# Optimization experiments

Measured on AMD Instinct MI355X. Metric: run time of the kernel, lower is better.

The kernel has to match this reference:

```python
import jax, jax.numpy as jnp
import numpy as np

WS = 7        # window size (cubic)
SHIFT = 3     # shift size (cubic)
NH = 6        # num heads
EPS = 1e-5


def _layernorm(x, g, b):
    m = x.mean(-1, keepdims=True)
    v = ((x - m) ** 2).mean(-1, keepdims=True)
    return (x - m) / jnp.sqrt(v + EPS) * g + b


def _win_partition(x, ws):
    # (B,H,W,T,C) -> (B*nW, ws^3, C)
    B, H, W, T, C = x.shape
    x = x.reshape(B, H // ws, ws, W // ws, ws, T // ws, ws, C)
    return x.transpose(0, 1, 3, 5, 2, 4, 6, 7).reshape(-1, ws * ws * ws, C)


def _win_reverse(w, ws, B, H, W, T):
    # (B*nW, ws^3, C) -> (B,H,W,T,C)
    C = w.shape[-1]
    x = w.reshape(B, H // ws, W // ws, T // ws, ws, ws, ws, C)
    return x.transpose(0, 1, 4, 2, 5, 3, 6, 7).reshape(B, H, W, T, C)


def _rel_index(ws):
    # 3D relative position index, (N, N) int, N = ws^3 (torch.meshgrid default 'ij')
    coords = np.stack(np.meshgrid(np.arange(ws), np.arange(ws), np.arange(ws), indexing='ij'))
    cf = coords.reshape(3, -1)
    rel = (cf[:, :, None] - cf[:, None, :]).transpose(1, 2, 0)
    rel[:, :, 0] += ws - 1
    rel[:, :, 1] += ws - 1
    rel[:, :, 2] += ws - 1
    rel[:, :, 0] *= (2 * ws - 1) ** 2
    rel[:, :, 1] *= (2 * ws - 1)
    return rel.sum(-1)


def _compute_mask(Hp, Wp, Tp, ws, shift):
    img = np.zeros((1, Hp, Wp, Tp, 1), np.float32)
    cnt = 0
    sl = (slice(0, -ws), slice(-ws, -shift), slice(-shift, None))
    for h in sl:
        for w in sl:
            for t in sl:
                img[:, h, w, t, :] = cnt
                cnt += 1
    mw = np.asarray(_win_partition(jnp.asarray(img), ws)).reshape(-1, ws ** 3)  # (nW, N)
    am = mw[:, None, :] - mw[:, :, None]
    return jnp.asarray(np.where(am != 0, -100.0, 0.0).astype(np.float32))


def setup_inputs() -> dict:
    key = jax.random.key(0)
    ks = jax.random.split(key, 10)
    B, Hd, Wd, Td, C = 2, 28, 28, 28, 192
    L = Hd * Wd * Td
    Ch = int(C * 4.0)
    s = 0.02
    inp = {
        'x': jax.random.normal(ks[0], (B, L, C), jnp.float32),
        'mask': _compute_mask(Hd, Wd, Td, WS, SHIFT),
        'gamma1': jnp.ones((C,), jnp.float32),
        'beta1': jnp.zeros((C,), jnp.float32),
        'qkv_w': jax.random.normal(ks[1], (3 * C, C), jnp.float32) * s,
        'qkv_b': jnp.zeros((3 * C,), jnp.float32),
        'rpb_table': jax.random.normal(ks[2], ((2 * WS - 1) ** 3, NH), jnp.float32) * s,
        'proj_w': jax.random.normal(ks[3], (C, C), jnp.float32) * s,
        'proj_b': jnp.zeros((C,), jnp.float32),
        'gamma2': jnp.ones((C,), jnp.float32),
        'beta2': jnp.zeros((C,), jnp.float32),
        'fc1_w': jax.random.normal(ks[4], (Ch, C), jnp.float32) * s,
        'fc1_b': jnp.zeros((Ch,), jnp.float32),
        'fc2_w': jax.random.normal(ks[5], (C, Ch), jnp.float32) * s,
        'fc2_b': jnp.zeros((C,), jnp.float32),
        'H': Hd, 'W': Wd, 'T': Td,
    }
    return inp


def reference(x, mask, gamma1, beta1, qkv_w, qkv_b, rpb_table, proj_w, proj_b,
              gamma2, beta2, fc1_w, fc1_b, fc2_w, fc2_b, H, W, T):
    B, L, C = x.shape
    hd = C // NH
    scale = hd ** -0.5
    shortcut = x

    h1 = _layernorm(x, gamma1, beta1).reshape(B, H, W, T, C)
    # H,W,T are multiples of WS -> no padding; cyclic shift for SW-MSA
    shifted = jnp.roll(h1, (-SHIFT, -SHIFT, -SHIFT), axis=(1, 2, 3))
    xw = _win_partition(shifted, WS)            # (B*nW, N, C)
    Bn, N, _ = xw.shape

    qkv = (xw @ qkv_w.T + qkv_b).reshape(Bn, N, 3, NH, hd).transpose(2, 0, 3, 1, 4)
    q, k, v = qkv[0] * scale, qkv[1], qkv[2]     # (Bn, NH, N, hd)
    attn = jnp.einsum('bhnd,bhmd->bhnm', q, k)   # (Bn, NH, N, N)

    idx = _rel_index(WS)
    bias = rpb_table[idx.reshape(-1)].reshape(N, N, NH).transpose(2, 0, 1)
    attn = attn + bias[None]

    nW = mask.shape[0]
    attn = attn.reshape(Bn // nW, nW, NH, N, N) + mask[None, :, None]
    attn = jax.nn.softmax(attn.reshape(Bn, NH, N, N), axis=-1)

    out = jnp.einsum('bhnm,bhmd->bhnd', attn, v).transpose(0, 2, 1, 3).reshape(Bn, N, C)
    out = out @ proj_w.T + proj_b

    shifted = _win_reverse(out, WS, B, H, W, T)
    xr = jnp.roll(shifted, (SHIFT, SHIFT, SHIFT), axis=(1, 2, 3)).reshape(B, L, C)

    x = shortcut + xr
    h2 = _layernorm(x, gamma2, beta2)
    m = jax.nn.gelu(h2 @ fc1_w.T + fc1_b, approximate=False)
    return x + (m @ fc2_w.T + fc2_b)
```

## Files before the change

kernel.cpp:

```cpp
#include <hip/hip_runtime.h>
#include <hip/hip_bf16.h>

typedef unsigned short u16;
typedef unsigned int u32;
typedef __attribute__((ext_vector_type(8))) short s16x8;
typedef __attribute__((ext_vector_type(4))) float f32x4;

__device__ __forceinline__ float bf2f(u16 v) {
    union { u32 u; float f; } x; x.u = ((u32)v) << 16; return x.f;
}
__device__ __forceinline__ u16 f2bf(float f) {
    union { float f; u32 u; } x; x.f = f;
    u32 r = x.u + 0x7fffu + ((x.u >> 16) & 1u);
    return (u16)(r >> 16);
}
__device__ __forceinline__ u32 f2bf_pk(float a, float b) {
    u32 ua = __builtin_bit_cast(u32, a);
    u32 ub = __builtin_bit_cast(u32, b);
    ua += 0x7fffu + ((ua >> 16) & 1u);
    ub += 0x7fffu + ((ub >> 16) & 1u);
    return __builtin_amdgcn_perm(ub, ua, 0x07060302);
}
__device__ __forceinline__ void gl2lds(const u16* g, u16* l) {
    __builtin_amdgcn_global_load_lds(
        (const __attribute__((address_space(1))) unsigned int*)g,
        (__attribute__((address_space(3))) unsigned int*)l, 16, 0, 0);
}

#define L_TOK 21952
#define C_DIM 192
#define LOG2E 1.4426950408889634f
#define Q2SCALE 0.2550565444463649f
#define BT_STR 352

__global__ __launch_bounds__(256) void cvt_k(const float* __restrict__ s0,
                                             const float* __restrict__ s1,
                                             const float* __restrict__ s2,
                                             const float* __restrict__ s3,
                                             u16* __restrict__ dst)
{
    int i = blockIdx.x * 256 + threadIdx.x;
    float v;
    if (i < 110592) v = s0[i];
    else if (i < 147456) v = s1[i - 110592];
    else if (i < 294912) v = s2[i - 147456];
    else v = s3[i - 294912];
    dst[i] = f2bf(v);
}

__global__ __launch_bounds__(256) void bias48_k(const float* __restrict__ rpb,
                                                u16* __restrict__ biasT)
{
    const int n = blockIdx.x * 256 + threadIdx.x;
    if (n >= BT_STR) return;
    const int m = blockIdx.y;
    const int z = blockIdx.z;
    const int hh = z >> 3, wt = z & 7;
    u16 v;
    if (n <= 342 && m <= 342) {
        int hq = n / 49, r1 = n - hq * 49, wq = r1 / 7, tq = r1 - wq * 7;
        int hm = m / 49, r2 = m - hm * 49, wm = r2 / 7, tm = r2 - wm * 7;
        int idx = ((hq - hm + 6) * 13 + (wq - wm + 6)) * 13 + (tq - tm + 6);
        float b = rpb[idx * 6 + hh];
        int rq = ((wt & 4) ? (hq < 4 ? 1 : 2) : 0) * 9
               + ((wt & 2) ? (wq < 4 ? 1 : 2) : 0) * 3
               + ((wt & 1) ? (tq < 4 ? 1 : 2) : 0);
        int rm = ((wt & 4) ? (hm < 4 ? 1 : 2) : 0) * 9
               + ((wt & 2) ? (wm < 4 ? 1 : 2) : 0) * 3
               + ((wt & 1) ? (tm < 4 ? 1 : 2) : 0);
        if (rq != rm) b -= 100.0f;
        v = f2bf(b * LOG2E);
    } else {
        v = f2bf(-100000.0f);
    }
    biasT[((size_t)z * 352 + m) * BT_STR + n] = v;
}

template<int MODE>
__global__ __launch_bounds__(256) void ln_k(const float* __restrict__ in,
                                            const float* __restrict__ g,
                                            const float* __restrict__ b,
                                            u16* __restrict__ out)
{
    const int lane = threadIdx.x & 63, wv = threadIdx.x >> 6;
    const int tok = blockIdx.x * 4 + wv;
    size_t base = (size_t)tok * C_DIM;
    float x0 = in[base + lane];
    float x1 = in[base + 64 + lane];
    float x2 = in[base + 128 + lane];
    float s = x0 + x1 + x2;
    float sq = x0 * x0 + x1 * x1 + x2 * x2;
    #pragma unroll
    for (int off = 32; off > 0; off >>= 1) {
        s += __shfl_xor(s, off, 64);
        sq += __shfl_xor(sq, off, 64);
    }
    const float mean = s * (1.0f / 192.0f);
    float var = sq * (1.0f / 192.0f) - mean * mean;
    var = fmaxf(var, 0.0f);
    const float rstd = rsqrtf(var + 1e-5f);

    size_t obase;
    if (MODE == 0) {
        int bi = tok / L_TOK;
        int l = tok - bi * L_TOK;
        int h = l / 784;
        int rm = l - h * 784;
        int w = rm / 28;
        int t = rm - w * 28;
        int hs = h + 25; if (hs >= 28) hs -= 28;
        int ws = w + 25; if (ws >= 28) ws -= 28;
        int ts = t + 25; if (ts >= 28) ts -= 28;
        int win = ((bi * 4 + hs / 7) * 4 + ws / 7) * 4 + ts / 7;
        int n = (hs % 7) * 49 + (ws % 7) * 7 + (ts % 7);
        obase = ((size_t)win * 343 + n) * C_DIM;
    } else {
        obase = base;
    }
    #pragma unroll
    for (int i = 0; i < 3; i++) {
        int c = lane + i * 64;
        float xv = (i == 0) ? x0 : (i == 1) ? x1 : x2;
        float y = (xv - mean) * rstd * g[c] + b[c];
        out[obase + c] = f2bf(y);
    }
}

template<int K, int EPI>
__global__ __launch_bounds__(256) void gemm_k(const u16* __restrict__ A,
                                              const u16* __restrict__ W,
                                              const float* __restrict__ bias,
                                              void* __restrict__ outp,
                                              const void* __restrict__ resp,
                                              int Ncols)
{
    __shared__ __align__(16) u16 As[3 * 128 * 32];
    __shared__ __align__(16) u16 Bs[3 * 64 * 32];
    const int t = threadIdx.x;
    const int bm = blockIdx.y;
    const int n0 = blockIdx.x * 64;
    const int lane = t & 63, wv = t >> 6;
    const int wm = (wv >> 1) * 64, wn = (wv & 1) * 32;
    const int r16 = lane & 15, quad = lane >> 4;

    f32x4 acc[4][2];
    #pragma unroll
    for (int i = 0; i < 4; i++)
        #pragma unroll
        for (int j = 0; j < 2; j++) acc[i][j] = (f32x4){0.f, 0.f, 0.f, 0.f};

    const int ar = t >> 2, ac = (t & 3) * 8;
    const size_t abase = (size_t)bm * 128 * K;

    for (int kc = 0; kc < K; kc += 96) {
        if (kc) __syncthreads();
        #pragma unroll
        for (int kt = 0; kt < 3; kt++) {
            const int k0 = kc + kt * 32;
            gl2lds(&A[abase + (size_t)ar * K + k0 + ac], &As[kt * 4096 + 8 * t]);
            gl2lds(&A[abase + (size_t)(ar + 64) * K + k0 + ac], &As[kt * 4096 + 2048 + 8 * t]);
            gl2lds(&W[(size_t)(n0 + ar) * K + k0 + ac], &Bs[kt * 2048 + 8 * t]);
        }
        __syncthreads();
        #pragma unroll
        for (int kt = 0; kt < 3; kt++) {
            s16x8 af[4], bf[2];
            #pragma unroll
            for (int fm = 0; fm < 4; fm++)
                af[fm] = *(const s16x8*)&As[kt * 4096 + (wm + fm * 16 + r16) * 32 + quad * 8];
            #pragma unroll
            for (int fn = 0; fn < 2; fn++)
                bf[fn] = *(const s16x8*)&Bs[kt * 2048 + (wn + fn * 16 + r16) * 32 + quad * 8];
            #pragma unroll
            for (int fm = 0; fm < 4; fm++)
                #pragma unroll
                for (int fn = 0; fn < 2; fn++)
                    acc[fm][fn] = __builtin_amdgcn_mfma_f32_16x16x32_bf16(af[fm], bf[fn], acc[fm][fn], 0, 0, 0);
        }
    }

    #pragma unroll
    for (int fm = 0; fm < 4; fm++) {
        #pragma unroll
        for (int fn = 0; fn < 2; fn++) {
            #pragma unroll
            for (int r = 0; r < 4; r++) {
                const int grow = bm * 128 + wm + fm * 16 + quad * 4 + r;
                const int gcol = n0 + wn + fn * 16 + r16;
                float v = acc[fm][fn][r] + bias[gcol];
                if (EPI == 0) {
                    if (gcol < 192) v *= Q2SCALE;
                    ((u16*)outp)[(size_t)grow * Ncols + gcol] = f2bf(v);
                } else if (EPI == 1) {
                    v = 0.5f * v * (1.0f + erff(v * 0.70710678118654752f));
                    ((u16*)outp)[(size_t)grow * Ncols + gcol] = f2bf(v);
                } else if (EPI == 2) {
                    size_t o = (size_t)grow * C_DIM + gcol;
                    ((float*)outp)[o] = v + ((const float*)resp)[o];
                } else {
                    int win = grow / 343, n = grow - win * 343;
                    int bi = win >> 6, wi = win & 63;
                    int hw = wi >> 4, ww = (wi >> 2) & 3, tw = wi & 3;
                    int ph = n / 49, rem = n - ph * 49;
                    int pw = rem / 7, pt = rem - pw * 7;
                    int h = hw * 7 + ph + 3; if (h >= 28) h -= 28;
                    int w = ww * 7 + pw + 3; if (w >= 28) w -= 28;
                    int tt = tw * 7 + pt + 3; if (tt >= 28) tt -= 28;
                    int l = (h * 28 + w) * 28 + tt;
                    size_t o = ((size_t)bi * L_TOK + l) * C_DIM + gcol;
                    ((float*)outp)[o] = v + ((const float*)resp)[o];
                }
            }
        }
    }
}

__global__ __launch_bounds__(256, 3) void attn_k(const u16* __restrict__ qkv,
                                                 const u16* __restrict__ biasAll,
                                                 u16* __restrict__ out)
{
    __shared__ __align__(16) u16 Ks[352 * 32];
    __shared__ __align__(16) u16 Vt[32 * 360];
    __shared__ __align__(16) u16 Pb[4][16 * 40];

    const int hh = blockIdx.x;
    const int win = blockIdx.y;
    const int wi = win & 63;
    const int t = threadIdx.x, lane = t & 63, wv = t >> 6;
    const int r16 = lane & 15, quad = lane >> 4;
    const size_t qbase = (size_t)win * 343 * 576 + hh * 32;

    for (int j = t; j < 343 * 4; j += 256) {
        int m = j >> 2, ch = j & 3;
        *(uint4*)&Ks[m * 32 + ch * 8] = *(const uint4*)&qkv[qbase + (size_t)m * 576 + 192 + ch * 8];
    }
    if (t < 36) {
        int m = 343 + (t >> 2), ch = t & 3;
        *(uint4*)&Ks[m * 32 + ch * 8] = (uint4){0u, 0u, 0u, 0u};
    }
    for (int i = t; i < 343 * 16; i += 256) {
        int m = i >> 4, d2 = (i & 15) * 2;
        int pm = (m & ~31) + 2 * (m & 15) + ((m >> 4) & 1);
        u32 w2 = *(const u32*)&qkv[qbase + (size_t)m * 576 + 384 + d2];
        Vt[d2 * 360 + pm] = (u16)(w2 & 0xffffu);
        Vt[(d2 + 1) * 360 + pm] = (u16)(w2 >> 16);
    }
    for (int i = t; i < 32 * 9; i += 256) {
        int d = i / 9, m = 343 + i % 9;
        int pm = (m & ~31) + 2 * (m & 15) + ((m >> 4) & 1);
        Vt[d * 360 + pm] = 0;
    }
    __syncthreads();

    const int wt = (((wi >> 4) == 3) ? 4 : 0) | ((((wi >> 2) & 3) == 3) ? 2 : 0)
                 | (((wi & 3) == 3) ? 1 : 0);
    const u16* biashT = biasAll + (size_t)(hh * 8 + wt) * 352 * BT_STR;

    for (int qt = 0; qt < 6; qt++) {
        const int row0 = qt * 64 + wv * 16;
        if (row0 > 342) continue;
        int qrow = row0 + r16; if (qrow > 342) qrow = 342;
        s16x8 qa = *(const s16x8*)&qkv[qbase + (size_t)qrow * 576 + quad * 8];

        const int n0 = row0 + quad * 4;

        f32x4 sacc[22];
        #pragma unroll
        for (int fn = 0; fn < 22; fn++) {
            const int col = fn * 16 + r16;
            uint2 bv = *(const uint2*)&biashT[(size_t)col * BT_STR + n0];
            sacc[fn][0] = bf2f((u16)(bv.x & 0xffffu));
            sacc[fn][1] = bf2f((u16)(bv.x >> 16));
            sacc[fn][2] = bf2f((u16)(bv.y & 0xffffu));
            sacc[fn][3] = bf2f((u16)(bv.y >> 16));
        }
        #pragma unroll
        for (int fn = 0; fn < 22; fn++) {
            s16x8 kb = *(const s16x8*)&Ks[(fn * 16 + r16) * 32 + quad * 8];
            sacc[fn] = __builtin_amdgcn_mfma_f32_16x16x32_bf16(qa, kb, sacc[fn], 0, 0, 0);
        }

        float rowsum[4] = {0.f, 0.f, 0.f, 0.f};
        #pragma unroll
        for (int fn = 0; fn < 22; fn++) {
            #pragma unroll
            for (int r = 0; r < 4; r++) {
                float p = exp2f(fminf(sacc[fn][r], 42.0f));
                sacc[fn][r] = p;
                rowsum[r] += p;
            }
        }
        #pragma unroll
        for (int r = 0; r < 4; r++) {
            float v = rowsum[r];
            #pragma unroll
            for (int off = 1; off < 16; off <<= 1) v += __shfl_xor(v, off, 64);
            rowsum[r] = v;
        }

        u16* pw = &Pb[wv][0];
        u32* pw32 = (u32*)pw;
        f32x4 oacc0 = (f32x4){0.f, 0.f, 0.f, 0.f};
        f32x4 oacc1 = (f32x4){0.f, 0.f, 0.f, 0.f};
        #pragma unroll
        for (int c = 0; c < 11; c++) {
            asm volatile("s_waitcnt lgkmcnt(0)" ::: "memory");
            #pragma unroll
            for (int r = 0; r < 4; r++)
                pw32[(quad * 4 + r) * 20 + r16] = f2bf_pk(sacc[2 * c][r], sacc[2 * c + 1][r]);
            asm volatile("s_waitcnt lgkmcnt(0)" ::: "memory");
            s16x8 pa = *(const s16x8*)&pw[r16 * 40 + quad * 8];
            s16x8 vb0 = *(const s16x8*)&Vt[r16 * 360 + c * 32 + quad * 8];
            s16x8 vb1 = *(const s16x8*)&Vt[(16 + r16) * 360 + c * 32 + quad * 8];
            oacc0 = __builtin_amdgcn_mfma_f32_16x16x32_bf16(pa, vb0, oacc0, 0, 0, 0);
            oacc1 = __builtin_amdgcn_mfma_f32_16x16x32_bf16(pa, vb1, oacc1, 0, 0, 0);
        }

        #pragma unroll
        for (int r = 0; r < 4; r++) {
            const int n = n0 + r;
            if (n < 343) {
                const float rs = rowsum[r];
                const float inv = rs > 0.0f ? 1.0f / rs : 0.0f;
                size_t o = ((size_t)win * 343 + n) * C_DIM + hh * 32;
                out[o + r16] = f2bf(oacc0[r] * inv);
                out[o + 16 + r16] = f2bf(oacc1[r] * inv);
            }
        }
    }
}

extern "C" void kernel_launch(void* const* d_in, const int* in_sizes, int n_in,
                              void* d_out, int out_size, void* d_ws, size_t ws_size,
                              hipStream_t stream)
{
    const float* x      = (const float*)d_in[0];
    const float* g1     = (const float*)d_in[2];
    const float* b1     = (const float*)d_in[3];
    const float* qkv_w  = (const float*)d_in[4];
    const float* qkv_b  = (const float*)d_in[5];
    const float* rpb    = (const float*)d_in[6];
    const float* proj_w = (const float*)d_in[7];
    const float* proj_b = (const float*)d_in[8];
    const float* g2     = (const float*)d_in[9];
    const float* b2     = (const float*)d_in[10];
    const float* fc1_w  = (const float*)d_in[11];
    const float* fc1_b  = (const float*)d_in[12];
    const float* fc2_w  = (const float*)d_in[13];
    const float* fc2_b  = (const float*)d_in[14];

    char* ws = (char*)d_ws;
    u16* xw        = (u16*)(ws + 0);
    u16* biasT     = (u16*)(ws + 0);
    u16* qkv       = (u16*)(ws + 16861184);
    u16* a1        = (u16*)(ws + 0);
    u16* attn_out  = (u16*)(ws + 67444736);
    u16* h2        = attn_out;
    float* x2      = (float*)(ws + 84305920);
    u16* wbf       = (u16*)(ws + 118028288);
    u16* qkv_wb = wbf;
    u16* proj_wb = wbf + 110592;
    u16* fc1_wb = wbf + 147456;
    u16* fc2_wb = wbf + 294912;

    cvt_k<<<dim3(1728), 256, 0, stream>>>(qkv_w, proj_w, fc1_w, fc2_w, wbf);
    ln_k<0><<<dim3(10976), 256, 0, stream>>>(x, g1, b1, xw);
    gemm_k<192, 0><<<dim3(9, 343), 256, 0, stream>>>(xw, qkv_wb, qkv_b, qkv, nullptr, 576);
    bias48_k<<<dim3(2, 352, 48), 256, 0, stream>>>(rpb, biasT);
    attn_k<<<dim3(6, 128), 256, 0, stream>>>(qkv, biasT, attn_out);
    gemm_k<192, 3><<<dim3(3, 343), 256, 0, stream>>>(attn_out, proj_wb, proj_b, x2, x, 192);
    ln_k<1><<<dim3(10976), 256, 0, stream>>>(x2, g2, b2, h2);
    gemm_k<192, 1><<<dim3(12, 343), 256, 0, stream>>>(h2, fc1_wb, fc1_b, a1, nullptr, 768);
    gemm_k<768, 2><<<dim3(3, 343), 256, 0, stream>>>(a1, fc2_wb, fc2_b, d_out, x2, 192);
}
```

Measured before the change: 360.4 us.

## Store attention bias as fp32, compute softmax row sums via MFMA, hardware bf16 pack

The precomputed bias table is now stored in fp32 and written four values at a time, so the attention kernel loads f32x4 directly into the score accumulators and no longer unpacks bf16. Softmax row sums now come from an extra MFMA against a ones vector inside the PV loop, which replaces the VALU adds and cross-lane shuffle reductions. The row sums are taken from the bf16-rounded probabilities, which keeps them consistent with the numerator. Manual bf16 rounding is replaced by the v_cvt_pk_bf16_f32 instruction. In exchange the bias table takes twice the memory traffic, and each chunk issues one more MFMA.

```diff
diff --git a/kernel.cpp b/kernel.cpp
--- a/kernel.cpp
+++ b/kernel.cpp
@@ -14,12 +14,10 @@
     u32 r = x.u + 0x7fffu + ((x.u >> 16) & 1u);
     return (u16)(r >> 16);
 }
-__device__ __forceinline__ u32 f2bf_pk(float a, float b) {
-    u32 ua = __builtin_bit_cast(u32, a);
-    u32 ub = __builtin_bit_cast(u32, b);
-    ua += 0x7fffu + ((ua >> 16) & 1u);
-    ub += 0x7fffu + ((ub >> 16) & 1u);
-    return __builtin_amdgcn_perm(ub, ua, 0x07060302);
+__device__ __forceinline__ u32 cvt_pk_bf16(float a, float b) {
+    u32 r;
+    asm("v_cvt_pk_bf16_f32 %0, %1, %2" : "=v"(r) : "v"(a), "v"(b));
+    return r;
 }
 __device__ __forceinline__ void gl2lds(const u16* g, u16* l) {
     __builtin_amdgcn_global_load_lds(
@@ -31,7 +29,7 @@
 #define C_DIM 192
 #define LOG2E 1.4426950408889634f
 #define Q2SCALE 0.2550565444463649f
-#define BT_STR 352
+#define BF_STR 352
 
 __global__ __launch_bounds__(256) void cvt_k(const float* __restrict__ s0,
                                              const float* __restrict__ s1,
@@ -49,31 +47,41 @@
 }
 
 __global__ __launch_bounds__(256) void bias48_k(const float* __restrict__ rpb,
-                                                u16* __restrict__ biasT)
-{
-    const int n = blockIdx.x * 256 + threadIdx.x;
-    if (n >= BT_STR) return;
-    const int m = blockIdx.y;
-    const int z = blockIdx.z;
+                                                float* __restrict__ biasF)
+{
+    const int gid = blockIdx.x * 256 + threadIdx.x;
+    const int z = gid / 30976;
+    const int rem = gid - z * 30976;
+    const int m = rem / 88;
+    const int n0 = (rem - m * 88) * 4;
     const int hh = z >> 3, wt = z & 7;
-    u16 v;
-    if (n <= 342 && m <= 342) {
-        int hq = n / 49, r1 = n - hq * 49, wq = r1 / 7, tq = r1 - wq * 7;
-        int hm = m / 49, r2 = m - hm * 49, wm = r2 / 7, tm = r2 - wm * 7;
-        int idx = ((hq - hm + 6) * 13 + (wq - wm + 6)) * 13 + (tq - tm + 6);
-        float b = rpb[idx * 6 + hh];
-        int rq = ((wt & 4) ? (hq < 4 ? 1 : 2) : 0) * 9
-               + ((wt & 2) ? (wq < 4 ? 1 : 2) : 0) * 3
-               + ((wt & 1) ? (tq < 4 ? 1 : 2) : 0);
-        int rm = ((wt & 4) ? (hm < 4 ? 1 : 2) : 0) * 9
-               + ((wt & 2) ? (wm < 4 ? 1 : 2) : 0) * 3
-               + ((wt & 1) ? (tm < 4 ? 1 : 2) : 0);
-        if (rq != rm) b -= 100.0f;
-        v = f2bf(b * LOG2E);
+
+    f32x4 vout;
+    if (m <= 342) {
+        const int hm = m / 49, r2 = m - hm * 49, wm = r2 / 7, tm = r2 - wm * 7;
+        const int rm = ((wt & 4) ? (hm < 4 ? 1 : 2) : 0) * 9
+                     + ((wt & 2) ? (wm < 4 ? 1 : 2) : 0) * 3
+                     + ((wt & 1) ? (tm < 4 ? 1 : 2) : 0);
+        #pragma unroll
+        for (int j = 0; j < 4; j++) {
+            const int n = n0 + j;
+            float v = -100000.0f;
+            if (n <= 342) {
+                int hq = n / 49, r1 = n - hq * 49, wq = r1 / 7, tq = r1 - wq * 7;
+                int idx = ((hq - hm + 6) * 13 + (wq - wm + 6)) * 13 + (tq - tm + 6);
+                float b = rpb[idx * 6 + hh];
+                int rq = ((wt & 4) ? (hq < 4 ? 1 : 2) : 0) * 9
+                       + ((wt & 2) ? (wq < 4 ? 1 : 2) : 0) * 3
+                       + ((wt & 1) ? (tq < 4 ? 1 : 2) : 0);
+                if (rq != rm) b -= 100.0f;
+                v = b * LOG2E;
+            }
+            vout[j] = v;
+        }
     } else {
-        v = f2bf(-100000.0f);
-    }
-    biasT[((size_t)z * 352 + m) * BT_STR + n] = v;
+        vout = (f32x4){-100000.0f, -100000.0f, -100000.0f, -100000.0f};
+    }
+    *(f32x4*)&biasF[((size_t)z * 352 + m) * BF_STR + n0] = vout;
 }
 
 template<int MODE>
@@ -216,7 +224,7 @@
 }
 
 __global__ __launch_bounds__(256, 3) void attn_k(const u16* __restrict__ qkv,
-                                                 const u16* __restrict__ biasAll,
+                                                 const float* __restrict__ biasAll,
                                                  u16* __restrict__ out)
 {
     __shared__ __align__(16) u16 Ks[352 * 32];
@@ -254,7 +262,11 @@
 
     const int wt = (((wi >> 4) == 3) ? 4 : 0) | ((((wi >> 2) & 3) == 3) ? 2 : 0)
                  | (((wi & 3) == 3) ? 1 : 0);
-    const u16* biashT = biasAll + (size_t)(hh * 8 + wt) * 352 * BT_STR;
+    const float* biashT = biasAll + (size_t)(hh * 8 + wt) * 352 * BF_STR;
+
+    s16x8 onesb;
+    #pragma unroll
+    for (int j = 0; j < 8; j++) onesb[j] = (short)0x3f80;
 
     for (int qt = 0; qt < 6; qt++) {
         const int row0 = qt * 64 + wv * 16;
@@ -268,11 +280,7 @@
         #pragma unroll
         for (int fn = 0; fn < 22; fn++) {
             const int col = fn * 16 + r16;
-            uint2 bv = *(const uint2*)&biashT[(size_t)col * BT_STR + n0];
-            sacc[fn][0] = bf2f((u16)(bv.x & 0xffffu));
-            sacc[fn][1] = bf2f((u16)(bv.x >> 16));
-            sacc[fn][2] = bf2f((u16)(bv.y & 0xffffu));
-            sacc[fn][3] = bf2f((u16)(bv.y >> 16));
+            sacc[fn] = *(const f32x4*)&biashT[(size_t)col * BF_STR + n0];
         }
         #pragma unroll
         for (int fn = 0; fn < 22; fn++) {
@@ -280,47 +288,38 @@
             sacc[fn] = __builtin_amdgcn_mfma_f32_16x16x32_bf16(qa, kb, sacc[fn], 0, 0, 0);
         }
 
-        float rowsum[4] = {0.f, 0.f, 0.f, 0.f};
         #pragma unroll
         for (int fn = 0; fn < 22; fn++) {
             #pragma unroll
-            for (int r = 0; r < 4; r++) {
-                float p = exp2f(fminf(sacc[fn][r], 42.0f));
-                sacc[fn][r] = p;
-                rowsum[r] += p;
-            }
-        }
-        #pragma unroll
-        for (int r = 0; r < 4; r++) {
-            float v = rowsum[r];
-            #pragma unroll
-            for (int off = 1; off < 16; off <<= 1) v += __shfl_xor(v, off, 64);
-            rowsum[r] = v;
+            for (int r = 0; r < 4; r++)
+                sacc[fn][r] = exp2f(fminf(sacc[fn][r], 42.0f));
         }
 
         u16* pw = &Pb[wv][0];
         u32* pw32 = (u32*)pw;
         f32x4 oacc0 = (f32x4){0.f, 0.f, 0.f, 0.f};
         f32x4 oacc1 = (f32x4){0.f, 0.f, 0.f, 0.f};
+        f32x4 osum  = (f32x4){0.f, 0.f, 0.f, 0.f};
         #pragma unroll
         for (int c = 0; c < 11; c++) {
             asm volatile("s_waitcnt lgkmcnt(0)" ::: "memory");
             #pragma unroll
             for (int r = 0; r < 4; r++)
-                pw32[(quad * 4 + r) * 20 + r16] = f2bf_pk(sacc[2 * c][r], sacc[2 * c + 1][r]);
+                pw32[(quad * 4 + r) * 20 + r16] = cvt_pk_bf16(sacc[2 * c][r], sacc[2 * c + 1][r]);
             asm volatile("s_waitcnt lgkmcnt(0)" ::: "memory");
             s16x8 pa = *(const s16x8*)&pw[r16 * 40 + quad * 8];
             s16x8 vb0 = *(const s16x8*)&Vt[r16 * 360 + c * 32 + quad * 8];
             s16x8 vb1 = *(const s16x8*)&Vt[(16 + r16) * 360 + c * 32 + quad * 8];
             oacc0 = __builtin_amdgcn_mfma_f32_16x16x32_bf16(pa, vb0, oacc0, 0, 0, 0);
             oacc1 = __builtin_amdgcn_mfma_f32_16x16x32_bf16(pa, vb1, oacc1, 0, 0, 0);
+            osum  = __builtin_amdgcn_mfma_f32_16x16x32_bf16(pa, onesb, osum, 0, 0, 0);
         }
 
         #pragma unroll
         for (int r = 0; r < 4; r++) {
             const int n = n0 + r;
             if (n < 343) {
-                const float rs = rowsum[r];
+                const float rs = osum[r];
                 const float inv = rs > 0.0f ? 1.0f / rs : 0.0f;
                 size_t o = ((size_t)win * 343 + n) * C_DIM + hh * 32;
                 out[o + r16] = f2bf(oacc0[r] * inv);
@@ -351,12 +350,12 @@
 
     char* ws = (char*)d_ws;
     u16* xw        = (u16*)(ws + 0);
-    u16* biasT     = (u16*)(ws + 0);
     u16* qkv       = (u16*)(ws + 16861184);
     u16* a1        = (u16*)(ws + 0);
     u16* attn_out  = (u16*)(ws + 67444736);
     u16* h2        = attn_out;
     float* x2      = (float*)(ws + 84305920);
+    float* biasF   = x2;
     u16* wbf       = (u16*)(ws + 118028288);
     u16* qkv_wb = wbf;
     u16* proj_wb = wbf + 110592;
@@ -366,8 +365,8 @@
     cvt_k<<<dim3(1728), 256, 0, stream>>>(qkv_w, proj_w, fc1_w, fc2_w, wbf);
     ln_k<0><<<dim3(10976), 256, 0, stream>>>(x, g1, b1, xw);
     gemm_k<192, 0><<<dim3(9, 343), 256, 0, stream>>>(xw, qkv_wb, qkv_b, qkv, nullptr, 576);
-    bias48_k<<<dim3(2, 352, 48), 256, 0, stream>>>(rpb, biasT);
-    attn_k<<<dim3(6, 128), 256, 0, stream>>>(qkv, biasT, attn_out);
+    bias48_k<<<dim3(5808), 256, 0, stream>>>(rpb, biasF);
+    attn_k<<<dim3(6, 128), 256, 0, stream>>>(qkv, biasF, attn_out);
     gemm_k<192, 3><<<dim3(3, 343), 256, 0, stream>>>(attn_out, proj_wb, proj_b, x2, x, 192);
     ln_k<1><<<dim3(10976), 256, 0, stream>>>(x2, g2, b2, h2);
     gemm_k<192, 1><<<dim3(12, 343), 256, 0, stream>>>(h2, fc1_wb, fc1_b, a1, nullptr, 768);
```

New measurement: 358.1 us. No clear change (-0.6%).
